# Kernel optimization log

Hardware: AMD Instinct MI355X
Metric: run time of the kernel (lower is better)

## Reference

```python
import jax, jax.numpy as jnp
import numpy as np

EMBED_DIM = 512
B, S, D = 4, 4096, EMBED_DIM

def setup_inputs() -> dict:
    key = jax.random.key(0)
    ks = jax.random.split(key, 11)
    s = 1.0 / np.sqrt(D)  # lecun-normal-ish init scale
    inp = {
        'k': jax.random.normal(ks[0], (B, S, D), jnp.float32),
        'v': jax.random.normal(ks[1], (B, S, D), jnp.float32),
        'q': jax.random.normal(ks[2], (B, S, D), jnp.float32),
        'Wk': jax.random.normal(ks[3], (D, D), jnp.float32) * s,
        'bk': jnp.zeros((D,), jnp.float32),
        'Wv': jax.random.normal(ks[4], (D, D), jnp.float32) * s,
        'bv': jnp.zeros((D,), jnp.float32),
        'Wq': jax.random.normal(ks[5], (D, D), jnp.float32) * s,
        'bq': jnp.zeros((D,), jnp.float32),
        'Wo': jax.random.normal(ks[6], (D, D), jnp.float32) * s,
        'bo': jnp.zeros((D,), jnp.float32),
    }
    return inp

def reference(k, v, q, Wk, bk, Wv, bv, Wq, bq, Wo, bo):
    # Dense projections: y = x @ W + b
    k_proj = k @ Wk + bk  # [B,S,D]
    v_proj = v @ Wv + bv
    q_proj = q @ Wq + bq
    # Full attention matrix (naive, as in original module)
    energy = jnp.einsum('bqd,bkd->bqk', q_proj, k_proj)  # [B,S,S]
    attention = jax.nn.softmax(energy / jnp.sqrt(jnp.asarray(EMBED_DIM, energy.dtype)), axis=-1)
    out = jnp.einsum('bqk,bkd->bqd', attention, v_proj)  # [B,S,D]
    linear_out = out @ Wo + bo
    return linear_out
```

## Files before the change

kernel.cpp:

```cpp
#include <hip/hip_runtime.h>
#include <hip/hip_bf16.h>


typedef __attribute__((ext_vector_type(8))) short bf16x8;
typedef __attribute__((ext_vector_type(4))) float f32x4;
typedef __attribute__((ext_vector_type(8))) unsigned short u16x8;

#define DEVI static __device__ __forceinline__

DEVI unsigned short f2b(float x) {
  __hip_bfloat16 h = __float2bfloat16(x);
  return __builtin_bit_cast(unsigned short, h);
}

typedef const void __attribute__((address_space(1)))* gptr_t;
typedef void __attribute__((address_space(3)))* lptr_t;

DEVI void gload_lds16(const void* g, void* l) {
  __builtin_amdgcn_global_load_lds((gptr_t)g, (lptr_t)l, 16, 0, 0);
}

__global__ void wtrans4_f32(const float* __restrict__ w0,
                            const float* __restrict__ w1,
                            const float* __restrict__ w2,
                            const float* __restrict__ w3,
                            unsigned short* __restrict__ WT) {
  __shared__ unsigned short s[32][33];
  const float* W = blockIdx.z == 0 ? w0 : (blockIdx.z == 1 ? w1
                   : (blockIdx.z == 2 ? w2 : w3));
  unsigned short* dst = WT + (long)blockIdx.z * 512 * 512;
  int tx = threadIdx.x, ty = threadIdx.y;
  int bx = blockIdx.x, by = blockIdx.y;
#pragma unroll
  for (int i = 0; i < 32; i += 8)
    s[ty + i][tx] = f2b(W[(by * 32 + ty + i) * 512 + bx * 32 + tx]);
  __syncthreads();
#pragma unroll
  for (int i = 0; i < 32; i += 8)
    dst[(bx * 32 + ty + i) * 512 + by * 32 + tx] = s[tx][ty + i];
}

__global__ __launch_bounds__(256) void reduce_partials(
    const float* __restrict__ part, float* __restrict__ rowsum, int nslot) {
  int r = blockIdx.x * 256 + threadIdx.x;
  float s = 0.f;
#pragma unroll 8
  for (int i = 0; i < nslot; ++i) s += part[(long)i * 16384 + r];
  rowsum[r] = s;
}

__global__ __launch_bounds__(256, 2) void proj_f32(
    const float* __restrict__ x0, const float* __restrict__ x1,
    const float* __restrict__ x2,
    const unsigned short* __restrict__ WT,
    unsigned short* __restrict__ Cout,
    const float* __restrict__ b0, const float* __restrict__ b1,
    const float* __restrict__ b2, int M) {
  const int K = 512, N = 512;
  __shared__ unsigned short As[2][128 * 64];
  __shared__ unsigned short Bs[2][128 * 64];

  const int gx = gridDim.x, gy = gridDim.y;
  const int nwg = gx * gy * gridDim.z;
  const int orig = (blockIdx.z * gy + blockIdx.y) * gx + blockIdx.x;
  const int qch = nwg >> 3;
  const int wg = (orig & 7) * qch + (orig >> 3);
  const int bx = wg % gx;
  const int tmp = wg / gx;
  const int by = tmp % gy;
  const int bz = tmp / gy;

  const float* Af = bz == 0 ? x0 : (bz == 1 ? x1 : x2);
  const unsigned short* Bb = WT + (long)bz * 512 * 512;
  const float* bias = bz == 0 ? b0 : (bz == 1 ? b1 : b2);

  const int t = threadIdx.x;
  const int lane = t & 63;
  const int wid = t >> 6;
  const int wr = wid >> 1, wc = wid & 1;
  const int lr = lane & 15, lk = lane >> 4;
  const long row0 = (long)by * 128;
  const long col0 = (long)bx * 128;
  const int r_ = t >> 3, c_ = t & 7;

  f32x4 acc[4][4] = {};
  float4 av[8];

  auto loadA = [&](int k0) {
#pragma unroll
    for (int p = 0; p < 4; ++p) {
      int r = p * 32 + r_;
      int cs = c_ ^ (r & 7);
      const float* src = Af + (row0 + r) * (long)K + k0 + cs * 8;
      av[2 * p] = *(const float4*)src;
      av[2 * p + 1] = *(const float4*)(src + 4);
    }
  };
  auto writeA = [&](int buf) {
#pragma unroll
    for (int p = 0; p < 4; ++p) {
      u16x8 o;
      o[0] = f2b(av[2 * p].x); o[1] = f2b(av[2 * p].y);
      o[2] = f2b(av[2 * p].z); o[3] = f2b(av[2 * p].w);
      o[4] = f2b(av[2 * p + 1].x); o[5] = f2b(av[2 * p + 1].y);
      o[6] = f2b(av[2 * p + 1].z); o[7] = f2b(av[2 * p + 1].w);
      *(u16x8*)((char*)As[buf] + (p * 256 + t) * 16) = o;
    }
  };
  auto stageB = [&](int buf, int k0) {
#pragma unroll
    for (int p = 0; p < 4; ++p) {
      int r = p * 32 + r_;
      int cs = c_ ^ (r & 7);
      gload_lds16(Bb + (col0 + r) * (long)K + k0 + cs * 8,
                  (char*)Bs[buf] + (p * 256 + t) * 16);
    }
  };

  const int nt = K >> 6;
  loadA(0);
  stageB(0, 0);
  writeA(0);
  asm volatile("s_waitcnt vmcnt(0)" ::: "memory");
  loadA(64);
  asm volatile("s_waitcnt lgkmcnt(0)" ::: "memory");
  int rd = 0;
  for (int tt = 0; tt < nt; ++tt) {
    if (tt + 1 < nt) {
      writeA(rd ^ 1);
      stageB(rd ^ 1, (tt + 1) << 6);
      if (tt + 2 < nt) loadA((tt + 2) << 6);
    } else {
      asm volatile("s_waitcnt vmcnt(0)" ::: "memory");
    }
    __builtin_amdgcn_sched_barrier(0);
    __builtin_amdgcn_s_barrier();
#pragma unroll
    for (int ks = 0; ks < 2; ++ks) {
      bf16x8 af[4], bfr[4];
#pragma unroll
      for (int mi = 0; mi < 4; ++mi) {
        int row = wr * 64 + mi * 16 + lr;
        int cc = (ks * 4 + lk) ^ (row & 7);
        af[mi] = *(const bf16x8*)((const char*)As[rd] + row * 128 + cc * 16);
      }
#pragma unroll
      for (int ni = 0; ni < 4; ++ni) {
        int row = wc * 64 + ni * 16 + lr;
        int cc = (ks * 4 + lk) ^ (row & 7);
        bfr[ni] = *(const bf16x8*)((const char*)Bs[rd] + row * 128 + cc * 16);
      }
#pragma unroll
      for (int mi = 0; mi < 4; ++mi)
#pragma unroll
        for (int ni = 0; ni < 4; ++ni)
          acc[mi][ni] = __builtin_amdgcn_mfma_f32_16x16x32_bf16(
              af[mi], bfr[ni], acc[mi][ni], 0, 0, 0);
    }
    asm volatile("s_waitcnt lgkmcnt(0)" ::: "memory");
    __builtin_amdgcn_s_barrier();
    rd ^= 1;
  }

  unsigned short* Cb = Cout + (long)bz * 8388608;
#pragma unroll
  for (int mi = 0; mi < 4; ++mi) {
#pragma unroll
    for (int ni = 0; ni < 4; ++ni) {
#pragma unroll
      for (int r = 0; r < 4; ++r) {
        long row = row0 + wr * 64 + mi * 16 + lk * 4 + r;
        long col = col0 + wc * 64 + ni * 16 + lr;
        Cb[row * N + col] = f2b(acc[mi][ni][r] + bias[col]);
      }
    }
  }
}

template <int EPI, bool HAS_BIAS>
__global__ __launch_bounds__(256, 2) void gemm_nt(
    const unsigned short* __restrict__ A,
    const unsigned short* __restrict__ B,
    void* __restrict__ Cv,
    const float* __restrict__ bias0,
    float* __restrict__ rowsum,
    int M, int N, int K, long sA, long sB, long sC) {
  __shared__ unsigned short As[2][128 * 64];
  __shared__ unsigned short Bs[2][128 * 64];

  const int gx = gridDim.x, gy = gridDim.y;
  const int nwg = gx * gy * gridDim.z;
  const int orig = (blockIdx.z * gy + blockIdx.y) * gx + blockIdx.x;
  const int qch = nwg >> 3;
  const int wg = (orig & 7) * qch + (orig >> 3);
  const int bx = wg % gx;
  const int tmp = wg / gx;
  const int by = tmp % gy;
  const int bz = tmp / gy;

  const unsigned short* Ab = A + (long)bz * sA;
  const unsigned short* Bb = B + (long)bz * sB;

  const int t = threadIdx.x;
  const int lane = t & 63;
  const int wid = t >> 6;
  const int wr = wid >> 1, wc = wid & 1;
  const int lr = lane & 15, lk = lane >> 4;
  const long row0 = (long)by * 128;
  const long col0 = (long)bx * 128;
  const int r_ = t >> 3, c_ = t & 7;

  f32x4 acc[4][4] = {};

  auto stage = [&](int buf, int k0) {
#pragma unroll
    for (int p = 0; p < 4; ++p) {
      int r = p * 32 + r_;
      int cs = c_ ^ (r & 7);
      gload_lds16(Ab + (row0 + r) * (long)K + k0 + cs * 8,
                  (char*)As[buf] + (p * 256 + t) * 16);
    }
#pragma unroll
    for (int p = 0; p < 4; ++p) {
      int r = p * 32 + r_;
      int cs = c_ ^ (r & 7);
      gload_lds16(Bb + (col0 + r) * (long)K + k0 + cs * 8,
                  (char*)Bs[buf] + (p * 256 + t) * 16);
    }
  };

  const int nt = K >> 6;
  stage(0, 0);
  int cur = 0;
  for (int tt = 0; tt < nt; ++tt) {
    if (tt + 1 < nt) {
      stage(cur ^ 1, (tt + 1) << 6);
      asm volatile("s_waitcnt vmcnt(8)" ::: "memory");
    } else {
      asm volatile("s_waitcnt vmcnt(0)" ::: "memory");
    }
    __builtin_amdgcn_s_barrier();
#pragma unroll
    for (int ks = 0; ks < 2; ++ks) {
      bf16x8 af[4], bfr[4];
#pragma unroll
      for (int mi = 0; mi < 4; ++mi) {
        int row = wr * 64 + mi * 16 + lr;
        int cc = (ks * 4 + lk) ^ (row & 7);
        af[mi] = *(const bf16x8*)((const char*)As[cur] + row * 128 + cc * 16);
      }
#pragma unroll
      for (int ni = 0; ni < 4; ++ni) {
        int row = wc * 64 + ni * 16 + lr;
        int cc = (ks * 4 + lk) ^ (row & 7);
        bfr[ni] = *(const bf16x8*)((const char*)Bs[cur] + row * 128 + cc * 16);
      }
#pragma unroll
      for (int mi = 0; mi < 4; ++mi)
#pragma unroll
        for (int ni = 0; ni < 4; ++ni)
          acc[mi][ni] = __builtin_amdgcn_mfma_f32_16x16x32_bf16(
              af[mi], bfr[ni], acc[mi][ni], 0, 0, 0);
    }
    asm volatile("s_waitcnt lgkmcnt(0)" ::: "memory");
    __builtin_amdgcn_s_barrier();
    cur ^= 1;
  }

  if constexpr (EPI == 2) {
#pragma unroll
    for (int mi = 0; mi < 4; ++mi) {
#pragma unroll
      for (int r = 0; r < 4; ++r) {
        long row = row0 + wr * 64 + mi * 16 + lk * 4 + r;
        float inv = 1.0f / rowsum[(long)bz * M + row];
#pragma unroll
        for (int ni = 0; ni < 4; ++ni) {
          long col = col0 + wc * 64 + ni * 16 + lr;
          float v = acc[mi][ni][r] * inv;
          if (HAS_BIAS) v += bias0[col];
          ((float*)Cv + bz * sC)[row * N + col] = v;
        }
      }
    }
  } else {
#pragma unroll
    for (int mi = 0; mi < 4; ++mi) {
#pragma unroll
      for (int ni = 0; ni < 4; ++ni) {
#pragma unroll
        for (int r = 0; r < 4; ++r) {
          long row = row0 + wr * 64 + mi * 16 + lk * 4 + r;
          long col = col0 + wc * 64 + ni * 16 + lr;
          float v = acc[mi][ni][r];
          if (HAS_BIAS) v += bias0[col];
          ((unsigned short*)Cv + bz * sC)[row * N + col] = f2b(v);
        }
      }
    }
  }
}

__global__ __launch_bounds__(512, 2) void gemm_e256(
    const unsigned short* __restrict__ A,
    const unsigned short* __restrict__ B,
    unsigned short* __restrict__ Cv,
    float* __restrict__ part,
    int M, int N, int K, long sA, long sB, long sC) {
  __shared__ unsigned short As[2][256 * 64];
  __shared__ unsigned short Bs[2][256 * 64];

  const int gx = gridDim.x, gy = gridDim.y;
  const int nwg = gx * gy * gridDim.z;
  const int orig = (blockIdx.z * gy + blockIdx.y) * gx + blockIdx.x;
  const int qch = nwg >> 3;
  const int wg = (orig & 7) * qch + (orig >> 3);
  const int bx = wg % gx;
  const int tmp = wg / gx;
  const int by = tmp % gy;
  const int bz = tmp / gy;

  const unsigned short* Ab = A + (long)bz * sA;
  const unsigned short* Bb = B + (long)bz * sB;

  const int t = threadIdx.x;
  const int lane = t & 63;
  const int wid = t >> 6;
  const int wrow = wid >> 2, wcol = wid & 3;
  const int lr = lane & 15, lk = lane >> 4;
  const long row0 = (long)by * 256;
  const long col0 = (long)bx * 256;

  f32x4 acc[8][4] = {};

  auto stage = [&](int buf, int k0) {
#pragma unroll
    for (int p = 0; p < 4; ++p) {
      int gg = p * 512 + t;
      int r = gg >> 3, c = gg & 7;
      gload_lds16(Ab + (row0 + r) * (long)K + k0 + (c ^ (r & 7)) * 8,
                  (char*)As[buf] + gg * 16);
    }
#pragma unroll
    for (int p = 0; p < 4; ++p) {
      int gg = p * 512 + t;
      int r = gg >> 3, c = gg & 7;
      gload_lds16(Bb + (col0 + r) * (long)K + k0 + (c ^ (r & 7)) * 8,
                  (char*)Bs[buf] + gg * 16);
    }
  };

  const int nt = K >> 6;
  stage(0, 0);
  asm volatile("s_waitcnt vmcnt(0)" ::: "memory");
  __builtin_amdgcn_s_barrier();

  int cur = 0;
  for (int tt = 0; tt < nt; ++tt) {
    if (tt + 1 < nt) stage(cur ^ 1, (tt + 1) << 6);
    __builtin_amdgcn_s_setprio(1);
#pragma unroll
    for (int s = 0; s < 2; ++s) {
      bf16x8 bfr[4];
#pragma unroll
      for (int n = 0; n < 4; ++n) {
        int rowB = wcol * 64 + n * 16 + lr;
        bfr[n] = *(const bf16x8*)((const char*)Bs[cur] + rowB * 128 +
                                  ((s * 4 + lk) ^ (rowB & 7)) * 16);
      }
#pragma unroll
      for (int h = 0; h < 2; ++h) {
        bf16x8 af[4];
#pragma unroll
        for (int m = 0; m < 4; ++m) {
          int rowA = wrow * 128 + (h * 4 + m) * 16 + lr;
          af[m] = *(const bf16x8*)((const char*)As[cur] + rowA * 128 +
                                   ((s * 4 + lk) ^ (rowA & 7)) * 16);
        }
#pragma unroll
        for (int m = 0; m < 4; ++m)
#pragma unroll
          for (int n = 0; n < 4; ++n)
            acc[h * 4 + m][n] = __builtin_amdgcn_mfma_f32_16x16x32_bf16(
                af[m], bfr[n], acc[h * 4 + m][n], 0, 0, 0);
      }
    }
    __builtin_amdgcn_s_setprio(0);
    asm volatile("s_waitcnt vmcnt(0)" ::: "memory");
    __builtin_amdgcn_sched_barrier(0);
    __builtin_amdgcn_s_barrier();
    cur ^= 1;
  }

  const float kScale = 0.04419417382415922f;
  const int slot = bx * 4 + wcol;
#pragma unroll
  for (int m = 0; m < 8; ++m) {
#pragma unroll
    for (int r = 0; r < 4; ++r) {
      long row = row0 + wrow * 128 + m * 16 + lk * 4 + r;
      float s = 0.f;
#pragma unroll
      for (int n = 0; n < 4; ++n) {
        long col = col0 + wcol * 64 + n * 16 + lr;
        float e = __expf(acc[m][n][r] * kScale);
        (Cv + bz * sC)[row * N + col] = f2b(e);
        s += e;
      }
      s += __shfl_xor(s, 1); s += __shfl_xor(s, 2);
      s += __shfl_xor(s, 4); s += __shfl_xor(s, 8);
      if ((lane & 15) == 0)
        part[(long)slot * 16384 + (long)bz * M + row] = s;
    }
  }
}

extern "C" void kernel_launch(void* const* d_in, const int* in_sizes, int n_in,
                              void* d_out, int out_size, void* d_ws, size_t ws_size,
                              hipStream_t stream) {
  const float* k_in = (const float*)d_in[0];
  const float* v_in = (const float*)d_in[1];
  const float* q_in = (const float*)d_in[2];
  const float* Wk = (const float*)d_in[3];
  const float* bk = (const float*)d_in[4];
  const float* Wv = (const float*)d_in[5];
  const float* bv = (const float*)d_in[6];
  const float* Wq = (const float*)d_in[7];
  const float* bq = (const float*)d_in[8];
  const float* Wo = (const float*)d_in[9];
  const float* bo = (const float*)d_in[10];

  const int B = 4, S = 4096, D = 512;
  const long BS = (long)B * S;
  const size_t MB = 1024 * 1024;
  if (ws_size < 226 * MB) return;

  char* ws = (char*)d_ws;
  unsigned short* P    = (unsigned short*)(ws + 0);
  unsigned short* KP   = (unsigned short*)(ws + 128 * MB);
  unsigned short* VP   = (unsigned short*)(ws + 144 * MB);
  unsigned short* QP   = (unsigned short*)(ws + 160 * MB);
  unsigned short* VWT  = (unsigned short*)(ws + 176 * MB);
  float* PART          = (float*)(ws + 192 * MB);
  float* ROWSUM        = (float*)(ws + 200 * MB);
  unsigned short* WTK  = (unsigned short*)(ws + 224 * MB);
  unsigned short* WTO  = WTK + 3L * 512 * 512;

  wtrans4_f32<<<dim3(16, 16, 4), dim3(32, 8), 0, stream>>>(
      Wk, Wv, Wq, Wo, WTK);

  proj_f32<<<dim3(D / 128, (int)(BS / 128), 3), 256, 0, stream>>>(
      k_in, v_in, q_in, WTK, KP, bk, bv, bq, (int)BS);

  gemm_nt<0, false><<<dim3(S / 128, D / 128, 4), 256, 0, stream>>>(
      WTO, VP, VWT, nullptr, nullptr, D, S, D,
      0, (long)S * D, (long)S * D);

  gemm_e256<<<dim3(S / 256, S / 256, 4), 512, 0, stream>>>(
      QP, KP, P, PART, S, S, D,
      (long)S * D, (long)S * D, (long)S * S);

  reduce_partials<<<64, 256, 0, stream>>>(PART, ROWSUM, 64);

  gemm_nt<2, true><<<dim3(D / 128, S / 128, 4), 256, 0, stream>>>(
      P, VWT, d_out, bo, ROWSUM, S, D, S,
      (long)S * S, (long)S * D, (long)S * D);
}
```

Measured before the change: 249.5 us.

## Fuse QK^T, exp, rowsum and PV into a single attention kernel

Replaces the separate score GEMM (which wrote a full bf16 exp(P) matrix), the partial-sum reduction and the final P·V GEMM with one fused kernel. Each block keeps a 64-row Q tile resident in LDS, streams K tiles through a double buffer, writes exponentiated scores to a small LDS tile, and accumulates P·V with V fragments read straight from global memory. Row sums are reduced across waves in LDS before normalising and adding the bias. This removes the large P write and read and two launches. In exchange it runs one 256-thread block per CU, synchronises at every K sub-step, and issues V loads without LDS staging or prefetch, so MFMA utilisation may suffer.

```diff
diff --git a/kernel.cpp b/kernel.cpp
--- a/kernel.cpp
+++ b/kernel.cpp
@@ -38,15 +38,6 @@
 #pragma unroll
   for (int i = 0; i < 32; i += 8)
     dst[(bx * 32 + ty + i) * 512 + by * 32 + tx] = s[tx][ty + i];
-}
-
-__global__ __launch_bounds__(256) void reduce_partials(
-    const float* __restrict__ part, float* __restrict__ rowsum, int nslot) {
-  int r = blockIdx.x * 256 + threadIdx.x;
-  float s = 0.f;
-#pragma unroll 8
-  for (int i = 0; i < nslot; ++i) s += part[(long)i * 16384 + r];
-  rowsum[r] = s;
 }
 
 __global__ __launch_bounds__(256, 2) void proj_f32(
@@ -177,13 +168,10 @@
   }
 }
 
-template <int EPI, bool HAS_BIAS>
 __global__ __launch_bounds__(256, 2) void gemm_nt(
     const unsigned short* __restrict__ A,
     const unsigned short* __restrict__ B,
-    void* __restrict__ Cv,
-    const float* __restrict__ bias0,
-    float* __restrict__ rowsum,
+    unsigned short* __restrict__ Cv,
     int M, int N, int K, long sA, long sB, long sC) {
   __shared__ unsigned short As[2][128 * 64];
   __shared__ unsigned short Bs[2][128 * 64];
@@ -267,150 +255,178 @@
     cur ^= 1;
   }
 
-  if constexpr (EPI == 2) {
-#pragma unroll
-    for (int mi = 0; mi < 4; ++mi) {
+#pragma unroll
+  for (int mi = 0; mi < 4; ++mi) {
+#pragma unroll
+    for (int ni = 0; ni < 4; ++ni) {
 #pragma unroll
       for (int r = 0; r < 4; ++r) {
         long row = row0 + wr * 64 + mi * 16 + lk * 4 + r;
-        float inv = 1.0f / rowsum[(long)bz * M + row];
-#pragma unroll
-        for (int ni = 0; ni < 4; ++ni) {
-          long col = col0 + wc * 64 + ni * 16 + lr;
-          float v = acc[mi][ni][r] * inv;
-          if (HAS_BIAS) v += bias0[col];
-          ((float*)Cv + bz * sC)[row * N + col] = v;
-        }
-      }
-    }
-  } else {
-#pragma unroll
-    for (int mi = 0; mi < 4; ++mi) {
-#pragma unroll
-      for (int ni = 0; ni < 4; ++ni) {
-#pragma unroll
-        for (int r = 0; r < 4; ++r) {
-          long row = row0 + wr * 64 + mi * 16 + lk * 4 + r;
-          long col = col0 + wc * 64 + ni * 16 + lr;
-          float v = acc[mi][ni][r];
-          if (HAS_BIAS) v += bias0[col];
-          ((unsigned short*)Cv + bz * sC)[row * N + col] = f2b(v);
-        }
-      }
-    }
-  }
-}
-
-__global__ __launch_bounds__(512, 2) void gemm_e256(
-    const unsigned short* __restrict__ A,
-    const unsigned short* __restrict__ B,
-    unsigned short* __restrict__ Cv,
-    float* __restrict__ part,
-    int M, int N, int K, long sA, long sB, long sC) {
-  __shared__ unsigned short As[2][256 * 64];
-  __shared__ unsigned short Bs[2][256 * 64];
-
-  const int gx = gridDim.x, gy = gridDim.y;
-  const int nwg = gx * gy * gridDim.z;
-  const int orig = (blockIdx.z * gy + blockIdx.y) * gx + blockIdx.x;
+        long col = col0 + wc * 64 + ni * 16 + lr;
+        (Cv + bz * sC)[row * N + col] = f2b(acc[mi][ni][r]);
+      }
+    }
+  }
+}
+
+__global__ __launch_bounds__(256, 1) void attn_fused(
+    const unsigned short* __restrict__ QP,
+    const unsigned short* __restrict__ KPB,
+    const unsigned short* __restrict__ VWT,
+    const float* __restrict__ bo,
+    float* __restrict__ out) {
+  const int S = 4096, D = 512;
+  __shared__ unsigned short qs[64 * 512];
+  __shared__ unsigned short ksb[2][128 * 64];
+  __shared__ unsigned short ps[64 * 128];
+  __shared__ float rsred[4][64];
+
+  const int gx = gridDim.x;
+  const int nwg = gx * gridDim.z;
+  const int orig = blockIdx.z * gx + blockIdx.x;
   const int qch = nwg >> 3;
   const int wg = (orig & 7) * qch + (orig >> 3);
   const int bx = wg % gx;
-  const int tmp = wg / gx;
-  const int by = tmp % gy;
-  const int bz = tmp / gy;
-
-  const unsigned short* Ab = A + (long)bz * sA;
-  const unsigned short* Bb = B + (long)bz * sB;
+  const int bz = wg / gx;
+
+  const long row0 = (long)bx * 64;
+  const unsigned short* Qb = QP + (long)bz * S * D;
+  const unsigned short* Kb = KPB + (long)bz * S * D;
+  const unsigned short* Vb = VWT + (long)bz * (long)D * S;
+  float* Ob = out + (long)bz * (long)S * D;
 
   const int t = threadIdx.x;
   const int lane = t & 63;
   const int wid = t >> 6;
-  const int wrow = wid >> 2, wcol = wid & 3;
   const int lr = lane & 15, lk = lane >> 4;
-  const long row0 = (long)by * 256;
-  const long col0 = (long)bx * 256;
-
-  f32x4 acc[8][4] = {};
-
-  auto stage = [&](int buf, int k0) {
-#pragma unroll
-    for (int p = 0; p < 4; ++p) {
-      int gg = p * 512 + t;
+
+#pragma unroll
+  for (int p = 0; p < 16; ++p) {
+    int gg = p * 256 + t;
+    int r = gg >> 6, c = gg & 63;
+    int cs = (c & 56) | ((c & 7) ^ (r & 7));
+    gload_lds16(Qb + (row0 + r) * (long)D + cs * 8, (char*)qs + gg * 16);
+  }
+  auto stageK = [&](int g) {
+    const unsigned short* src = Kb + (long)((g >> 3) * 128) * D + (g & 7) * 64;
+#pragma unroll
+    for (int p = 0; p < 4; ++p) {
+      int gg = p * 256 + t;
       int r = gg >> 3, c = gg & 7;
-      gload_lds16(Ab + (row0 + r) * (long)K + k0 + (c ^ (r & 7)) * 8,
-                  (char*)As[buf] + gg * 16);
-    }
-#pragma unroll
-    for (int p = 0; p < 4; ++p) {
-      int gg = p * 512 + t;
-      int r = gg >> 3, c = gg & 7;
-      gload_lds16(Bb + (col0 + r) * (long)K + k0 + (c ^ (r & 7)) * 8,
-                  (char*)Bs[buf] + gg * 16);
+      gload_lds16(src + (long)r * D + (c ^ (r & 7)) * 8,
+                  (char*)ksb[g & 1] + gg * 16);
     }
   };
-
-  const int nt = K >> 6;
-  stage(0, 0);
+  stageK(0);
   asm volatile("s_waitcnt vmcnt(0)" ::: "memory");
   __builtin_amdgcn_s_barrier();
 
-  int cur = 0;
-  for (int tt = 0; tt < nt; ++tt) {
-    if (tt + 1 < nt) stage(cur ^ 1, (tt + 1) << 6);
-    __builtin_amdgcn_s_setprio(1);
-#pragma unroll
-    for (int s = 0; s < 2; ++s) {
-      bf16x8 bfr[4];
-#pragma unroll
-      for (int n = 0; n < 4; ++n) {
-        int rowB = wcol * 64 + n * 16 + lr;
-        bfr[n] = *(const bf16x8*)((const char*)Bs[cur] + rowB * 128 +
-                                  ((s * 4 + lk) ^ (rowB & 7)) * 16);
-      }
-#pragma unroll
-      for (int h = 0; h < 2; ++h) {
-        bf16x8 af[4];
+  f32x4 oacc[4][8] = {};
+  float rs[4][4] = {};
+  const float kScale = 0.04419417382415922f;
+
+  for (int kt = 0; kt < 32; ++kt) {
+    f32x4 eacc[4][2] = {};
+    for (int kk = 0; kk < 8; ++kk) {
+      const int g = kt * 8 + kk;
+      if (g + 1 < 256) {
+        stageK(g + 1);
+        asm volatile("s_waitcnt vmcnt(4)" ::: "memory");
+      } else {
+        asm volatile("s_waitcnt vmcnt(0)" ::: "memory");
+      }
+      __builtin_amdgcn_s_barrier();
+#pragma unroll
+      for (int s = 0; s < 2; ++s) {
+        bf16x8 af[4], bf2[2];
 #pragma unroll
         for (int m = 0; m < 4; ++m) {
-          int rowA = wrow * 128 + (h * 4 + m) * 16 + lr;
-          af[m] = *(const bf16x8*)((const char*)As[cur] + rowA * 128 +
-                                   ((s * 4 + lk) ^ (rowA & 7)) * 16);
+          int row = m * 16 + lr;
+          int ch = kk * 8 + ((s * 4 + lk) ^ (row & 7));
+          af[m] = *(const bf16x8*)((const char*)qs + row * 1024 + ch * 16);
         }
 #pragma unroll
+        for (int n = 0; n < 2; ++n) {
+          int col = wid * 32 + n * 16 + lr;
+          int ch = (s * 4 + lk) ^ (col & 7);
+          bf2[n] = *(const bf16x8*)((const char*)ksb[g & 1] + col * 128 +
+                                    ch * 16);
+        }
+#pragma unroll
         for (int m = 0; m < 4; ++m)
 #pragma unroll
-          for (int n = 0; n < 4; ++n)
-            acc[h * 4 + m][n] = __builtin_amdgcn_mfma_f32_16x16x32_bf16(
-                af[m], bfr[n], acc[h * 4 + m][n], 0, 0, 0);
-      }
-    }
-    __builtin_amdgcn_s_setprio(0);
-    asm volatile("s_waitcnt vmcnt(0)" ::: "memory");
-    __builtin_amdgcn_sched_barrier(0);
+          for (int n = 0; n < 2; ++n)
+            eacc[m][n] = __builtin_amdgcn_mfma_f32_16x16x32_bf16(
+                af[m], bf2[n], eacc[m][n], 0, 0, 0);
+      }
+      asm volatile("s_waitcnt lgkmcnt(0)" ::: "memory");
+      __builtin_amdgcn_s_barrier();
+    }
+#pragma unroll
+    for (int m = 0; m < 4; ++m) {
+#pragma unroll
+      for (int r = 0; r < 4; ++r) {
+        int row = m * 16 + lk * 4 + r;
+#pragma unroll
+        for (int n = 0; n < 2; ++n) {
+          float e = __expf(eacc[m][n][r] * kScale);
+          rs[m][r] += e;
+          int colE = wid * 32 + n * 16 + lr;
+          int ch = (colE >> 3) ^ (row & 7);
+          *(unsigned short*)((char*)ps + row * 256 + ch * 16 +
+                             (colE & 7) * 2) = f2b(e);
+        }
+      }
+    }
+    asm volatile("s_waitcnt lgkmcnt(0)" ::: "memory");
     __builtin_amdgcn_s_barrier();
-    cur ^= 1;
-  }
-
-  const float kScale = 0.04419417382415922f;
-  const int slot = bx * 4 + wcol;
-#pragma unroll
-  for (int m = 0; m < 8; ++m) {
+#pragma unroll
+    for (int ks = 0; ks < 4; ++ks) {
+      bf16x8 af[4], bv[8];
+#pragma unroll
+      for (int m = 0; m < 4; ++m) {
+        int row = m * 16 + lr;
+        int ch = (ks * 4 + lk) ^ (row & 7);
+        af[m] = *(const bf16x8*)((const char*)ps + row * 256 + ch * 16);
+      }
+#pragma unroll
+      for (int n = 0; n < 8; ++n) {
+        int col = wid * 128 + n * 16 + lr;
+        bv[n] = *(const bf16x8*)(Vb + (long)col * S + kt * 128 + ks * 32 +
+                                 lk * 8);
+      }
+#pragma unroll
+      for (int m = 0; m < 4; ++m)
+#pragma unroll
+        for (int n = 0; n < 8; ++n)
+          oacc[m][n] = __builtin_amdgcn_mfma_f32_16x16x32_bf16(
+              af[m], bv[n], oacc[m][n], 0, 0, 0);
+    }
+  }
+
+#pragma unroll
+  for (int m = 0; m < 4; ++m) {
 #pragma unroll
     for (int r = 0; r < 4; ++r) {
-      long row = row0 + wrow * 128 + m * 16 + lk * 4 + r;
-      float s = 0.f;
-#pragma unroll
-      for (int n = 0; n < 4; ++n) {
-        long col = col0 + wcol * 64 + n * 16 + lr;
-        float e = __expf(acc[m][n][r] * kScale);
-        (Cv + bz * sC)[row * N + col] = f2b(e);
-        s += e;
-      }
+      float s = rs[m][r];
       s += __shfl_xor(s, 1); s += __shfl_xor(s, 2);
       s += __shfl_xor(s, 4); s += __shfl_xor(s, 8);
-      if ((lane & 15) == 0)
-        part[(long)slot * 16384 + (long)bz * M + row] = s;
+      if (lr == 0) rsred[wid][m * 16 + lk * 4 + r] = s;
+    }
+  }
+  __syncthreads();
+#pragma unroll
+  for (int m = 0; m < 4; ++m) {
+#pragma unroll
+    for (int r = 0; r < 4; ++r) {
+      int row = m * 16 + lk * 4 + r;
+      float inv = 1.0f / (rsred[0][row] + rsred[1][row] +
+                          rsred[2][row] + rsred[3][row]);
+#pragma unroll
+      for (int n = 0; n < 8; ++n) {
+        int col = wid * 128 + n * 16 + lr;
+        Ob[(row0 + row) * (long)D + col] = oacc[m][n][r] * inv + bo[col];
+      }
     }
   }
 }
@@ -436,13 +452,10 @@
   if (ws_size < 226 * MB) return;
 
   char* ws = (char*)d_ws;
-  unsigned short* P    = (unsigned short*)(ws + 0);
   unsigned short* KP   = (unsigned short*)(ws + 128 * MB);
   unsigned short* VP   = (unsigned short*)(ws + 144 * MB);
   unsigned short* QP   = (unsigned short*)(ws + 160 * MB);
   unsigned short* VWT  = (unsigned short*)(ws + 176 * MB);
-  float* PART          = (float*)(ws + 192 * MB);
-  float* ROWSUM        = (float*)(ws + 200 * MB);
   unsigned short* WTK  = (unsigned short*)(ws + 224 * MB);
   unsigned short* WTO  = WTK + 3L * 512 * 512;
 
@@ -452,17 +465,9 @@
   proj_f32<<<dim3(D / 128, (int)(BS / 128), 3), 256, 0, stream>>>(
       k_in, v_in, q_in, WTK, KP, bk, bv, bq, (int)BS);
 
-  gemm_nt<0, false><<<dim3(S / 128, D / 128, 4), 256, 0, stream>>>(
-      WTO, VP, VWT, nullptr, nullptr, D, S, D,
-      0, (long)S * D, (long)S * D);
-
-  gemm_e256<<<dim3(S / 256, S / 256, 4), 512, 0, stream>>>(
-      QP, KP, P, PART, S, S, D,
-      (long)S * D, (long)S * D, (long)S * S);
-
-  reduce_partials<<<64, 256, 0, stream>>>(PART, ROWSUM, 64);
-
-  gemm_nt<2, true><<<dim3(D / 128, S / 128, 4), 256, 0, stream>>>(
-      P, VWT, d_out, bo, ROWSUM, S, D, S,
-      (long)S * S, (long)S * D, (long)S * D);
-}
+  gemm_nt<<<dim3(S / 128, D / 128, 4), 256, 0, stream>>>(
+      WTO, VP, VWT, D, S, D, 0, (long)S * D, (long)S * D);
+
+  attn_fused<<<dim3(S / 64, 1, 4), 256, 0, stream>>>(
+      QP, KP, VWT, bo, (float*)d_out);
+}
```

New measurement: 337.3 us. 35.2% more time.
